# Performance work log

Measured on AMD Instinct MI355X. Metric: run time of the kernel, lower is better.

Reference implementation:

```python
import jax, jax.numpy as jnp
import numpy as np

B, S, H = 2, 2048, 2048
NH, NKV, HD = 32, 4, 128
THETA = 1e6
EPS = 1e-6


def setup_inputs() -> dict:
    key = jax.random.key(0)
    ks = jax.random.split(key, 6)
    scale = 0.02
    hidden_states = jax.random.normal(ks[0], (B, S, H), jnp.float32)
    attention_mask = jnp.broadcast_to(jnp.tril(jnp.ones((S, S), bool))[None, None], (B, 1, S, S))
    position_ids = jnp.broadcast_to(jnp.arange(S, dtype=jnp.int32), (B, S))
    Wq = jax.random.normal(ks[1], (H, NH * HD), jnp.float32) * scale
    Wk = jax.random.normal(ks[2], (H, NKV * HD), jnp.float32) * scale
    Wv = jax.random.normal(ks[3], (H, NKV * HD), jnp.float32) * scale
    Wo = jax.random.normal(ks[4], (NH * HD, H), jnp.float32) * scale
    q_norm_w = jnp.ones((HD,), jnp.float32)
    k_norm_w = jnp.ones((HD,), jnp.float32)
    return dict(hidden_states=hidden_states, attention_mask=attention_mask,
                position_ids=position_ids, Wq=Wq, Wk=Wk, Wv=Wv, Wo=Wo,
                q_norm_w=q_norm_w, k_norm_w=k_norm_w)


def _rms_norm(x, w):
    # per-head RMSNorm over last dim (head_dim)
    var = jnp.mean(x * x, axis=-1, keepdims=True)
    return x * jax.lax.rsqrt(var + EPS) * w


def _rotate_half(x):
    x1, x2 = jnp.split(x, 2, axis=-1)
    return jnp.concatenate([-x2, x1], axis=-1)


def _rope(position_ids):
    inv_freq = 1.0 / (THETA ** (jnp.arange(0, HD, 2, dtype=jnp.float32) / HD))  # [HD/2]
    freqs = position_ids.astype(jnp.float32)[..., None] * inv_freq  # [B,S,HD/2]
    emb = jnp.concatenate([freqs, freqs], axis=-1)  # [B,S,HD]
    return jnp.cos(emb), jnp.sin(emb)


def reference(hidden_states, attention_mask, position_ids, Wq, Wk, Wv, Wo, q_norm_w, k_norm_w):
    cos, sin = _rope(position_ids)               # [B,S,HD]
    cos = cos[:, :, None, :]                     # [B,S,1,HD] broadcast over heads
    sin = sin[:, :, None, :]

    q = (hidden_states @ Wq).reshape(B, S, NH, HD)
    k = (hidden_states @ Wk).reshape(B, S, NKV, HD)
    v = (hidden_states @ Wv).reshape(B, S, NKV, HD)

    q = _rms_norm(q, q_norm_w)
    k = _rms_norm(k, k_norm_w)

    q = q * cos + _rotate_half(q) * sin
    k = k * cos + _rotate_half(k) * sin

    # GQA: repeat each kv head NH//NKV times (matches HF repeat_kv ordering)
    k = jnp.repeat(k, NH // NKV, axis=2)         # [B,S,NH,HD]
    v = jnp.repeat(v, NH // NKV, axis=2)

    q = q.transpose(0, 2, 1, 3)                  # [B,NH,S,HD]
    k = k.transpose(0, 2, 1, 3)
    v = v.transpose(0, 2, 1, 3)

    scores = jnp.einsum('bhqd,bhkd->bhqk', q, k) * (HD ** -0.5)
    scores = jnp.where(attention_mask, scores, jnp.finfo(scores.dtype).min)
    attn = jax.nn.softmax(scores, axis=-1)
    ctx = jnp.einsum('bhqk,bhkd->bhqd', attn, v)  # [B,NH,S,HD]
    ctx = ctx.transpose(0, 2, 1, 3).reshape(B, S, NH * HD)
    return ctx @ Wo                               # [B,S,H]
```

## Files before the change

### kernel.cpp

```cpp
#include <hip/hip_runtime.h>
#include <stdint.h>
#include <stddef.h>

typedef unsigned short ushort_t;
typedef unsigned int uint32;

typedef _Float16 half8 __attribute__((ext_vector_type(8)));
typedef _Float16 half4 __attribute__((ext_vector_type(4)));
typedef float f32x4 __attribute__((ext_vector_type(4)));

#define NLINV (-0.2158673600755816f)
#define INV2PI 0.15915494309189535f
#define TWOPI 6.283185307179586f
#define FPITCH 40

#define GLDS(gptr, lptr)                                                                   \
  __builtin_amdgcn_global_load_lds((const __attribute__((address_space(1))) unsigned int*)(gptr), \
                                   (__attribute__((address_space(3))) unsigned int*)(lptr), \
                                   16, 0, 0)

static __device__ __forceinline__ float bf_lo(uint32 u) { union { uint32 u; float f; } v; v.u = u << 16; return v.f; }
static __device__ __forceinline__ float bf_hi(uint32 u) { union { uint32 u; float f; } v; v.u = u & 0xffff0000u; return v.f; }
static __device__ __forceinline__ ushort_t f2bf(float f) {
  union { float f; uint32 u; } v; v.f = f;
  return (ushort_t)((v.u + 0x7fffu + ((v.u >> 16) & 1u)) >> 16);
}
static __device__ __forceinline__ half8 cvt8(uint4 u) {
  half8 h;
  h[0] = (_Float16)bf_lo(u.x); h[1] = (_Float16)bf_hi(u.x);
  h[2] = (_Float16)bf_lo(u.y); h[3] = (_Float16)bf_hi(u.y);
  h[4] = (_Float16)bf_lo(u.z); h[5] = (_Float16)bf_hi(u.z);
  h[6] = (_Float16)bf_lo(u.w); h[7] = (_Float16)bf_hi(u.w);
  return h;
}
static __device__ __forceinline__ half8 load8h(const void* p, int mode, size_t eidx) {
  if (mode == 2) return ((const half8*)p)[eidx >> 3];
  if (mode == 1) {
    const float4* q = (const float4*)p + (eidx >> 2);
    const float4 a = q[0], b = q[1];
    half8 h;
    h[0] = (_Float16)a.x; h[1] = (_Float16)a.y; h[2] = (_Float16)a.z; h[3] = (_Float16)a.w;
    h[4] = (_Float16)b.x; h[5] = (_Float16)b.y; h[6] = (_Float16)b.z; h[7] = (_Float16)b.w;
    return h;
  }
  return cvt8(((const uint4*)p)[eidx >> 3]);
}
static __device__ __forceinline__ float wval(const void* w, int is_f32, int i) {
  if (is_f32) return ((const float*)w)[i];
  union { uint32 u; float f; } v; v.u = ((uint32)((const ushort_t*)w)[i]) << 16; return v.f;
}
static __device__ __forceinline__ int probe_f32(const void* p) {
  const uint32 u = ((const uint32*)p)[threadIdx.x & 63];
  const int e = (u >> 7) & 0xff;
  return __popcll(__ballot(e >= 110 && e <= 135)) < 32 ? 1 : 0;
}

__global__ __launch_bounds__(256) void probe_fill(uint32* out, uint32 pat, int nwords) {
  for (int i = blockIdx.x * 256 + threadIdx.x; i < nwords; i += gridDim.x * 256) out[i] = pat;
}

__global__ __launch_bounds__(256) void convert_hs(const void* __restrict__ hs,
                                                  _Float16* __restrict__ hsF, int n8) {
  const int f = probe_f32(hs);
  for (int i = blockIdx.x * 256 + threadIdx.x; i < n8; i += gridDim.x * 256)
    ((half8*)hsF)[i] = load8h(hs, f, (size_t)i << 3);
}

__global__ __launch_bounds__(256) void transpose_w(const void* __restrict__ W, int K, int N,
                                                   _Float16* __restrict__ Wt) {
  __shared__ __align__(16) _Float16 T[64][72];
  const int fw = probe_f32(W);
  const int n0 = blockIdx.x * 64, k0 = blockIdx.y * 64;
  const int tid = threadIdx.x;
  const int r = tid >> 2, cc = (tid & 3) * 16;
  const size_t src = (size_t)(k0 + r) * N + n0 + cc;
  const half8 v0 = load8h(W, fw, src);
  const half8 v1 = load8h(W, fw, src + 8);
  *(half8*)&T[r][cc] = v0;
  *(half8*)&T[r][cc + 8] = v1;
  __syncthreads();
  half8 o0, o1;
#pragma unroll
  for (int j = 0; j < 8; ++j) { o0[j] = T[cc + j][r]; o1[j] = T[cc + 8 + j][r]; }
  _Float16* dst = Wt + (size_t)(n0 + r) * K + k0 + cc;
  *(half8*)dst = o0;
  *(half8*)(dst + 8) = o1;
}


__global__ __launch_bounds__(256) void gemm2_rope(const _Float16* __restrict__ Af, int lda,
                                                  int arow0, const _Float16* __restrict__ Bt,
                                                  int ldb, _Float16* __restrict__ C, int ldc,
                                                  int K, const void* __restrict__ w) {
  __shared__ __align__(16) _Float16 As[128 * 32];
  __shared__ __align__(16) _Float16 Bs[128 * 32];
  __shared__ float Ct[64 * 128];
  const int fw = probe_f32(w);
  const int tid = threadIdx.x;
  const int wave = tid >> 6, lane = tid & 63;
  const int m0 = blockIdx.y * 128, n0 = blockIdx.x * 128;
  const int wm = (wave >> 1) * 64, wn = (wave & 1) * 64;
  const int fr = lane & 15, quad = lane >> 4;
  const int r0 = wave * 32 + (lane >> 2);
  const int r1 = r0 + 16;
  const int cs0 = ((lane & 3) ^ ((r0 >> 1) & 3)) << 3;
  const int cs1 = ((lane & 3) ^ ((r1 >> 1) & 3)) << 3;
  const _Float16* Ar0 = Af + (size_t)(arow0 + m0 + r0) * lda + cs0;
  const _Float16* Ar1 = Af + (size_t)(arow0 + m0 + r1) * lda + cs1;
  const _Float16* Br0 = Bt + (size_t)(n0 + r0) * ldb + cs0;
  const _Float16* Br1 = Bt + (size_t)(n0 + r1) * ldb + cs1;
  _Float16* lA0 = &As[(wave * 32) * 32];
  _Float16* lA1 = &As[(wave * 32 + 16) * 32];
  _Float16* lB0 = &Bs[(wave * 32) * 32];
  _Float16* lB1 = &Bs[(wave * 32 + 16) * 32];
  f32x4 acc[4][4] = {};
  for (int k0 = 0; k0 < K; k0 += 32) {
    __syncthreads();
    GLDS(Ar0 + k0, lA0);
    GLDS(Ar1 + k0, lA1);
    GLDS(Br0 + k0, lB0);
    GLDS(Br1 + k0, lB1);
    __syncthreads();
    half8 a[4], b[4];
#pragma unroll
    for (int t = 0; t < 4; ++t) {
      const int row = wm + t * 16 + fr;
      a[t] = *(const half8*)&As[row * 32 + ((quad ^ ((row >> 1) & 3)) << 3)];
    }
#pragma unroll
    for (int t = 0; t < 4; ++t) {
      const int row = wn + t * 16 + fr;
      b[t] = *(const half8*)&Bs[row * 32 + ((quad ^ ((row >> 1) & 3)) << 3)];
    }
#pragma unroll
    for (int mt = 0; mt < 4; ++mt)
#pragma unroll
      for (int nt = 0; nt < 4; ++nt)
        acc[mt][nt] = __builtin_amdgcn_mfma_f32_16x16x32_f16(a[mt], b[nt], acc[mt][nt], 0, 0, 0);
  }
  __syncthreads();
#pragma unroll
  for (int hf = 0; hf < 2; ++hf) {
    if ((wave >> 1) == hf) {
#pragma unroll
      for (int mt = 0; mt < 4; ++mt)
#pragma unroll
        for (int nt = 0; nt < 4; ++nt)
#pragma unroll
          for (int r = 0; r < 4; ++r)
            Ct[(mt * 16 + quad * 4 + r) * 128 + wn + nt * 16 + fr] = acc[mt][nt][r];
    }
    __syncthreads();
    const int row = tid >> 2, sub = tid & 3;
    float ss = 0.f;
#pragma unroll
    for (int j = 0; j < 32; ++j) {
      const float v = Ct[row * 128 + sub * 32 + j];
      ss += v * v;
    }
    ss += __shfl_xor(ss, 1);
    ss += __shfl_xor(ss, 2);
    const float rinv = rsqrtf(ss * (1.0f / 128.0f) + 1e-6f);
    const int grow = m0 + hf * 64 + row;
    const int s = (arow0 + grow) & 2047;
    uint32 obuf[16];
#pragma unroll
    for (int j = 0; j < 32; j += 2) {
      float o2[2];
#pragma unroll
      for (int e = 0; e < 2; ++e) {
        const int c = sub * 32 + j + e;
        const float x = Ct[row * 128 + c];
        const float p = Ct[row * 128 + (c ^ 64)];
        const float xn = x * rinv * wval(w, fw, c);
        const float pn = p * rinv * wval(w, fw, c ^ 64);
        const float rot = (c < 64) ? -pn : pn;
        const float fq = __expf((float)(c & 63) * NLINV);
        float rev = (float)s * fq * INV2PI;
        rev -= rintf(rev);
        float sn, cs;
        __sincosf(rev * TWOPI, &sn, &cs);
        o2[e] = xn * cs + rot * sn;
      }
      union { _Float16 h[2]; uint32 u; } pk;
      pk.h[0] = (_Float16)o2[0]; pk.h[1] = (_Float16)o2[1];
      obuf[j >> 1] = pk.u;
    }
    uint32* dst = (uint32*)(C + (size_t)grow * ldc + n0 + sub * 32);
#pragma unroll
    for (int j2 = 0; j2 < 16; ++j2) dst[j2] = obuf[j2];
    __syncthreads();
  }
}

__global__ __launch_bounds__(256) void gemm2_plain(const _Float16* __restrict__ Af, int lda,
                                                   int arow0, const _Float16* __restrict__ Bt,
                                                   int ldb, char* __restrict__ obase,
                                                   size_t oeoff, int ldc, int omode, int K,
                                                   const void* __restrict__ pES) {
  __shared__ __align__(16) _Float16 As[128 * 32];
  __shared__ __align__(16) _Float16 Bs[128 * 32];
  const int fes = probe_f32(pES);
  const int tid = threadIdx.x;
  const int wave = tid >> 6, lane = tid & 63;
  const int m0 = blockIdx.y * 128, n0 = blockIdx.x * 128;
  const int wm = (wave >> 1) * 64, wn = (wave & 1) * 64;
  const int fr = lane & 15, quad = lane >> 4;
  const int r0 = wave * 32 + (lane >> 2);
  const int r1 = r0 + 16;
  const int cs0 = ((lane & 3) ^ ((r0 >> 1) & 3)) << 3;
  const int cs1 = ((lane & 3) ^ ((r1 >> 1) & 3)) << 3;
  const _Float16* Ar0 = Af + (size_t)(arow0 + m0 + r0) * lda + cs0;
  const _Float16* Ar1 = Af + (size_t)(arow0 + m0 + r1) * lda + cs1;
  const _Float16* Br0 = Bt + (size_t)(n0 + r0) * ldb + cs0;
  const _Float16* Br1 = Bt + (size_t)(n0 + r1) * ldb + cs1;
  _Float16* lA0 = &As[(wave * 32) * 32];
  _Float16* lA1 = &As[(wave * 32 + 16) * 32];
  _Float16* lB0 = &Bs[(wave * 32) * 32];
  _Float16* lB1 = &Bs[(wave * 32 + 16) * 32];
  f32x4 acc[4][4] = {};
  for (int k0 = 0; k0 < K; k0 += 32) {
    __syncthreads();
    GLDS(Ar0 + k0, lA0);
    GLDS(Ar1 + k0, lA1);
    GLDS(Br0 + k0, lB0);
    GLDS(Br1 + k0, lB1);
    __syncthreads();
    half8 a[4], b[4];
#pragma unroll
    for (int t = 0; t < 4; ++t) {
      const int row = wm + t * 16 + fr;
      a[t] = *(const half8*)&As[row * 32 + ((quad ^ ((row >> 1) & 3)) << 3)];
    }
#pragma unroll
    for (int t = 0; t < 4; ++t) {
      const int row = wn + t * 16 + fr;
      b[t] = *(const half8*)&Bs[row * 32 + ((quad ^ ((row >> 1) & 3)) << 3)];
    }
#pragma unroll
    for (int mt = 0; mt < 4; ++mt)
#pragma unroll
      for (int nt = 0; nt < 4; ++nt)
        acc[mt][nt] = __builtin_amdgcn_mfma_f32_16x16x32_f16(a[mt], b[nt], acc[mt][nt], 0, 0, 0);
  }
  if (omode == 2) {
#pragma unroll
    for (int mt = 0; mt < 4; ++mt)
#pragma unroll
      for (int nt = 0; nt < 4; ++nt) {
        half4 pk;
#pragma unroll
        for (int r = 0; r < 4; ++r) pk[r] = (_Float16)acc[mt][nt][r];
        *(half4*)((_Float16*)obase + (size_t)(n0 + wn + nt * 16 + fr) * ldc +
                  m0 + wm + mt * 16 + quad * 4) = pk;
      }
    return;
  }
#pragma unroll
  for (int mt = 0; mt < 4; ++mt)
#pragma unroll
    for (int nt = 0; nt < 4; ++nt)
#pragma unroll
      for (int r = 0; r < 4; ++r) {
        const size_t idx = (size_t)(m0 + wm + mt * 16 + quad * 4 + r) * ldc + n0 + wn + nt * 16 + fr;
        const float v = acc[mt][nt][r];
        if (fes) ((float*)obase)[oeoff + idx] = v;
        else ((ushort_t*)obase)[oeoff + idx] = f2bf(v);
      }
}

__global__ __launch_bounds__(256) void gemm_rope_fast(const void* __restrict__ Araw, int lda,
                                                      int arow0, const _Float16* __restrict__ Bt,
                                                      int ldb, char* __restrict__ obase,
                                                      size_t oeoff, int ldc, int K,
                                                      const void* __restrict__ w) {
  __shared__ __align__(16) _Float16 As[128 * FPITCH];
  __shared__ __align__(16) _Float16 Bs[128 * FPITCH];
  __shared__ float Ct[64 * 128];
  const int fa = probe_f32(Araw);
  const int fw = probe_f32(w);
  _Float16* Cv = (_Float16*)(obase + oeoff * (fa ? 4u : 2u));
  const int tid = threadIdx.x;
  const int wave = tid >> 6, lane = tid & 63;
  const int m0 = blockIdx.y * 128, n0 = blockIdx.x * 128;
  const int wm = (wave >> 1) * 64, wn = (wave & 1) * 64;
  const int fr = lane & 15, quad = lane >> 4;
  const int sr = tid >> 1, sc = (tid & 1) * 16;
  f32x4 acc[4][4] = {};
  for (int k0 = 0; k0 < K; k0 += 32) {
    const size_t aidx = (size_t)(arow0 + m0 + sr) * lda + k0 + sc;
    const half8 av0 = load8h(Araw, fa, aidx);
    const half8 av1 = load8h(Araw, fa, aidx + 8);
    const _Float16* bp = Bt + (size_t)(n0 + sr) * ldb + k0 + sc;
    const half8 bv0 = *(const half8*)bp;
    const half8 bv1 = *(const half8*)(bp + 8);
    __syncthreads();
    *(half8*)&As[sr * FPITCH + sc] = av0;
    *(half8*)&As[sr * FPITCH + sc + 8] = av1;
    *(half8*)&Bs[sr * FPITCH + sc] = bv0;
    *(half8*)&Bs[sr * FPITCH + sc + 8] = bv1;
    __syncthreads();
    half8 a[4], b[4];
#pragma unroll
    for (int t = 0; t < 4; ++t)
      a[t] = *(const half8*)&As[(wm + t * 16 + fr) * FPITCH + quad * 8];
#pragma unroll
    for (int t = 0; t < 4; ++t)
      b[t] = *(const half8*)&Bs[(wn + t * 16 + fr) * FPITCH + quad * 8];
#pragma unroll
    for (int mt = 0; mt < 4; ++mt)
#pragma unroll
      for (int nt = 0; nt < 4; ++nt)
        acc[mt][nt] = __builtin_amdgcn_mfma_f32_16x16x32_f16(a[mt], b[nt], acc[mt][nt], 0, 0, 0);
  }
  __syncthreads();
#pragma unroll
  for (int hf = 0; hf < 2; ++hf) {
    if ((wave >> 1) == hf) {
#pragma unroll
      for (int mt = 0; mt < 4; ++mt)
#pragma unroll
        for (int nt = 0; nt < 4; ++nt)
#pragma unroll
          for (int r = 0; r < 4; ++r)
            Ct[(mt * 16 + quad * 4 + r) * 128 + wn + nt * 16 + fr] = acc[mt][nt][r];
    }
    __syncthreads();
    const int row = tid >> 2, sub = tid & 3;
    float ss = 0.f;
#pragma unroll
    for (int j = 0; j < 32; ++j) {
      const float v = Ct[row * 128 + sub * 32 + j];
      ss += v * v;
    }
    ss += __shfl_xor(ss, 1);
    ss += __shfl_xor(ss, 2);
    const float rinv = rsqrtf(ss * (1.0f / 128.0f) + 1e-6f);
    const int grow = m0 + hf * 64 + row;
    const int s = (arow0 + grow) & 2047;
    uint32 obuf[16];
#pragma unroll
    for (int j = 0; j < 32; j += 2) {
      float o2[2];
#pragma unroll
      for (int e = 0; e < 2; ++e) {
        const int c = sub * 32 + j + e;
        const float x = Ct[row * 128 + c];
        const float p = Ct[row * 128 + (c ^ 64)];
        const float xn = x * rinv * wval(w, fw, c);
        const float pn = p * rinv * wval(w, fw, c ^ 64);
        const float rot = (c < 64) ? -pn : pn;
        const float fq = __expf((float)(c & 63) * NLINV);
        float rev = (float)s * fq * INV2PI;
        rev -= rintf(rev);
        float sn, cs;
        __sincosf(rev * TWOPI, &sn, &cs);
        o2[e] = xn * cs + rot * sn;
      }
      union { _Float16 h[2]; uint32 u; } pk;
      pk.h[0] = (_Float16)o2[0]; pk.h[1] = (_Float16)o2[1];
      obuf[j >> 1] = pk.u;
    }
    uint32* dst = (uint32*)(Cv + (size_t)grow * ldc + n0 + sub * 32);
#pragma unroll
    for (int j2 = 0; j2 < 16; ++j2) dst[j2] = obuf[j2];
    __syncthreads();
  }
}

__global__ __launch_bounds__(256) void gemm_plain_fast(const char* __restrict__ abase, size_t aeoff,
                                                       int lda, int amode, int arow0,
                                                       const _Float16* __restrict__ Bt, int ldb,
                                                       char* __restrict__ obase, size_t oeoff,
                                                       int ldc, int omode, int K,
                                                       const void* __restrict__ pES) {
  __shared__ __align__(16) _Float16 As[128 * FPITCH];
  __shared__ __align__(16) _Float16 Bs[128 * FPITCH];
  const int fes = probe_f32(pES);
  const uint32 es = fes ? 4u : 2u;
  const void* A = abase + aeoff * es;
  const int fa = (amode == 2) ? 2 : probe_f32(abase);
  const int tid = threadIdx.x;
  const int wave = tid >> 6, lane = tid & 63;
  const int m0 = blockIdx.y * 128, n0 = blockIdx.x * 128;
  const int wm = (wave >> 1) * 64, wn = (wave & 1) * 64;
  const int fr = lane & 15, quad = lane >> 4;
  const int sr = tid >> 1, sc = (tid & 1) * 16;
  f32x4 acc[4][4] = {};
  for (int k0 = 0; k0 < K; k0 += 32) {
    const size_t aidx = (size_t)(arow0 + m0 + sr) * lda + k0 + sc;
    const half8 av0 = load8h(A, fa, aidx);
    const half8 av1 = load8h(A, fa, aidx + 8);
    const _Float16* bp = Bt + (size_t)(n0 + sr) * ldb + k0 + sc;
    const half8 bv0 = *(const half8*)bp;
    const half8 bv1 = *(const half8*)(bp + 8);
    __syncthreads();
    *(half8*)&As[sr * FPITCH + sc] = av0;
    *(half8*)&As[sr * FPITCH + sc + 8] = av1;
    *(half8*)&Bs[sr * FPITCH + sc] = bv0;
    *(half8*)&Bs[sr * FPITCH + sc + 8] = bv1;
    __syncthreads();
    half8 a[4], b[4];
#pragma unroll
    for (int t = 0; t < 4; ++t)
      a[t] = *(const half8*)&As[(wm + t * 16 + fr) * FPITCH + quad * 8];
#pragma unroll
    for (int t = 0; t < 4; ++t)
      b[t] = *(const half8*)&Bs[(wn + t * 16 + fr) * FPITCH + quad * 8];
#pragma unroll
    for (int mt = 0; mt < 4; ++mt)
#pragma unroll
      for (int nt = 0; nt < 4; ++nt)
        acc[mt][nt] = __builtin_amdgcn_mfma_f32_16x16x32_f16(a[mt], b[nt], acc[mt][nt], 0, 0, 0);
  }
  if (omode == 2) {
#pragma unroll
    for (int mt = 0; mt < 4; ++mt)
#pragma unroll
      for (int nt = 0; nt < 4; ++nt) {
        half4 pk;
#pragma unroll
        for (int r = 0; r < 4; ++r) pk[r] = (_Float16)acc[mt][nt][r];
        *(half4*)((_Float16*)obase + (size_t)(n0 + wn + nt * 16 + fr) * ldc +
                  m0 + wm + mt * 16 + quad * 4) = pk;
      }
    return;
  }
#pragma unroll
  for (int mt = 0; mt < 4; ++mt)
#pragma unroll
    for (int nt = 0; nt < 4; ++nt)
#pragma unroll
      for (int r = 0; r < 4; ++r) {
        const size_t idx = (size_t)(m0 + wm + mt * 16 + quad * 4 + r) * ldc + n0 + wn + nt * 16 + fr;
        const float v = acc[mt][nt][r];
        if (omode == 1) ((_Float16*)obase)[idx] = (_Float16)v;
        else if (fes) ((float*)obase)[oeoff + idx] = v;
        else ((ushort_t*)obase)[oeoff + idx] = f2bf(v);
      }
}

#define LOADKV(J0)                                                                             \
  {                                                                                            \
    _Pragma("unroll") for (int ii = 0; ii < 4; ++ii) {                                         \
      const int i = tid + ii * 256;                                                            \
      const int r = i >> 4, c = i & 15;                                                        \
      kreg[ii] = *(const half8*)(Kb + (size_t)((J0) + r) * 512 + kv * 128 + ((c ^ (r & 7)) << 3)); \
      const int d = i >> 3, c2 = i & 7;                                                        \
      vreg[ii] = *(const half8*)(Vb + (size_t)(kv * 128 + d) * 2048 + (J0) + ((c2 ^ (d & 7)) << 3)); \
    }                                                                                          \
  }

__global__ __launch_bounds__(256, 2) void attn_fwd(char* __restrict__ qbase, size_t qeoff,
                                                   const _Float16* __restrict__ Kb,
                                                   const _Float16* __restrict__ Vb, int c0,
                                                   const void* __restrict__ pES) {
  __shared__ __align__(16) _Float16 Ks[64 * 128];
  __shared__ __align__(16) _Float16 Vt[128 * 64];
  __shared__ __align__(16) _Float16 Ps[4 * 16 * 64];
  const uint32 es = probe_f32(pES) ? 4u : 2u;
  _Float16* Qbuf = (_Float16*)(qbase + qeoff * es);
  const int tid = threadIdx.x;
  const int wave = tid >> 6, lane = tid & 63;
  const int fr = lane & 15, quad = lane >> 4;
  const int h = blockIdx.y, kv = h >> 3;
  const int qb0 = blockIdx.x * 64;
  const int qg = c0 + qb0;
  const int qrow0 = qb0 + wave * 16;
  _Float16* Pw = &Ps[wave * 1024];
  half8 qa[4];
#pragma unroll
  for (int kt = 0; kt < 4; ++kt)
    qa[kt] = *(const half8*)(Qbuf + (size_t)(qrow0 + fr) * 4096 + h * 128 + kt * 32 + quad * 8);
  f32x4 Oa[8];
#pragma unroll
  for (int dt = 0; dt < 8; ++dt) Oa[dt] = (f32x4)0.f;
  float mr[4], lr[4];
#pragma unroll
  for (int r = 0; r < 4; ++r) { mr[r] = -1e30f; lr[r] = 0.f; }
  const int ntiles = qg / 64 + 1;
  half8 kreg[4], vreg[4];
  LOADKV(0);
  for (int t = 0; t < ntiles; ++t) {
    __syncthreads();
#pragma unroll
    for (int ii = 0; ii < 4; ++ii) {
      *(half8*)&Ks[(tid + ii * 256) * 8] = kreg[ii];
      *(half8*)&Vt[(tid + ii * 256) * 8] = vreg[ii];
    }
    __syncthreads();
    if (t + 1 < ntiles) LOADKV((t + 1) * 64);
    f32x4 s[4];
#pragma unroll
    for (int nt = 0; nt < 4; ++nt) s[nt] = (f32x4)0.f;
#pragma unroll
    for (int kt = 0; kt < 4; ++kt)
#pragma unroll
      for (int nt = 0; nt < 4; ++nt) {
        const int row = nt * 16 + fr;
        const int boff = ((row << 8) + ((kt * 32 + quad * 8) << 1)) ^ ((row & 7) << 4);
        const half8 kb = *(const half8*)((const char*)Ks + boff);
        s[nt] = __builtin_amdgcn_mfma_f32_16x16x32_f16(qa[kt], kb, s[nt], 0, 0, 0);
      }
    const float SC = 0.08838834764831845f;
    const int j0 = t * 64;
    if (t == ntiles - 1) {
#pragma unroll
      for (int nt = 0; nt < 4; ++nt)
#pragma unroll
        for (int r = 0; r < 4; ++r) {
          const int kpos = j0 + nt * 16 + fr;
          const int qpos = qg + wave * 16 + quad * 4 + r;
          s[nt][r] = (kpos > qpos) ? -1e30f : s[nt][r] * SC;
        }
    } else {
#pragma unroll
      for (int nt = 0; nt < 4; ++nt)
#pragma unroll
        for (int r = 0; r < 4; ++r) s[nt][r] *= SC;
    }
    float al[4];
#pragma unroll
    for (int r = 0; r < 4; ++r) {
      float mx = fmaxf(fmaxf(s[0][r], s[1][r]), fmaxf(s[2][r], s[3][r]));
      mx = fmaxf(mx, __shfl_xor(mx, 1));
      mx = fmaxf(mx, __shfl_xor(mx, 2));
      mx = fmaxf(mx, __shfl_xor(mx, 4));
      mx = fmaxf(mx, __shfl_xor(mx, 8));
      const float mn = fmaxf(mr[r], mx);
      al[r] = __expf(mr[r] - mn);
      mr[r] = mn;
    }
    float rs[4] = {0.f, 0.f, 0.f, 0.f};
#pragma unroll
    for (int nt = 0; nt < 4; ++nt)
#pragma unroll
      for (int r = 0; r < 4; ++r) {
        const float p = __expf(s[nt][r] - mr[r]);
        rs[r] += p;
        const int q = quad * 4 + r;
        const int boff = (((q << 7) + ((nt * 16 + fr) << 1)) ^ ((q & 7) << 4));
        *(_Float16*)((char*)Pw + boff) = (_Float16)p;
      }
#pragma unroll
    for (int r = 0; r < 4; ++r) {
      rs[r] += __shfl_xor(rs[r], 1);
      rs[r] += __shfl_xor(rs[r], 2);
      rs[r] += __shfl_xor(rs[r], 4);
      rs[r] += __shfl_xor(rs[r], 8);
      lr[r] = lr[r] * al[r] + rs[r];
    }
#pragma unroll
    for (int dt = 0; dt < 8; ++dt)
#pragma unroll
      for (int r = 0; r < 4; ++r) Oa[dt][r] *= al[r];
    half8 pa[2];
#pragma unroll
    for (int kt = 0; kt < 2; ++kt) {
      const int boff = (((fr << 7) + ((kt * 32 + quad * 8) << 1)) ^ ((fr & 7) << 4));
      pa[kt] = *(const half8*)((const char*)Pw + boff);
    }
#pragma unroll
    for (int dt = 0; dt < 8; ++dt)
#pragma unroll
      for (int kt = 0; kt < 2; ++kt) {
        const int d = dt * 16 + fr;
        const int boff = (((d << 7) + ((kt * 32 + quad * 8) << 1)) ^ ((d & 7) << 4));
        const half8 vb = *(const half8*)((const char*)Vt + boff);
        Oa[dt] = __builtin_amdgcn_mfma_f32_16x16x32_f16(pa[kt], vb, Oa[dt], 0, 0, 0);
      }
  }
#pragma unroll
  for (int r = 0; r < 4; ++r) {
    const float linv = 1.0f / lr[r];
    _Float16* orow = Qbuf + (size_t)(qrow0 + quad * 4 + r) * 4096 + h * 128;
#pragma unroll
    for (int dt = 0; dt < 8; ++dt) orow[dt * 16 + fr] = (_Float16)(Oa[dt][r] * linv);
  }
}

extern "C" void kernel_launch(void* const* d_in, const int* in_sizes, int n_in,
                              void* d_out, int out_size, void* d_ws, size_t ws_size,
                              hipStream_t stream) {
  (void)in_sizes; (void)n_in; (void)out_size;
  const void* hs = d_in[0];
  const void* Wq = d_in[3];
  const void* Wk = d_in[4];
  const void* Wv = d_in[5];
  const void* Wo = d_in[6];
  const void* qw = d_in[7];
  const void* kw = d_in[8];
  char* dout = (char*)d_out;
  const size_t MB = 1048576;

  probe_fill<<<2048, 256, 0, stream>>>((uint32*)d_out, 0x42C842C8u, 4194304);
  if (ws_size < 40 * MB) {
    probe_fill<<<2048, 256, 0, stream>>>((uint32*)d_out, 0x43484348u, 4194304);
    return;
  }
  _Float16* Kbuf = (_Float16*)d_ws;
  _Float16* Vbuf = (_Float16*)((char*)d_ws + 2 * MB);
  _Float16* WqT = (_Float16*)((char*)d_ws + 4 * MB);
  _Float16* WoT = (_Float16*)((char*)d_ws + 20 * MB);
  _Float16* WkT = (_Float16*)((char*)d_ws + 36 * MB);
  _Float16* WvT = (_Float16*)((char*)d_ws + 38 * MB);
  const size_t QOFF = 4194304;

  transpose_w<<<dim3(64, 32), 256, 0, stream>>>(Wq, 2048, 4096, WqT);
  transpose_w<<<dim3(8, 32), 256, 0, stream>>>(Wk, 2048, 512, WkT);
  transpose_w<<<dim3(8, 32), 256, 0, stream>>>(Wv, 2048, 512, WvT);
  transpose_w<<<dim3(32, 64), 256, 0, stream>>>(Wo, 4096, 2048, WoT);

  if (ws_size >= 72 * MB) {
    char* Qw = (char*)d_ws + 40 * MB;
    _Float16* hsF = (_Float16*)((char*)d_ws + 56 * MB);
    convert_hs<<<2048, 256, 0, stream>>>(hs, hsF, 1048576);
    for (int b = 0; b < 2; ++b) {
      gemm2_rope<<<dim3(4, 16), 256, 0, stream>>>(hsF, 2048, b * 2048, WkT, 2048,
                                                  Kbuf, 512, 2048, kw);
      gemm2_plain<<<dim3(4, 16), 256, 0, stream>>>(hsF, 2048, b * 2048, WvT, 2048,
                                                   (char*)Vbuf, 0, 2048, 2, 2048, hs);
      gemm2_rope<<<dim3(32, 16), 256, 0, stream>>>(hsF, 2048, b * 2048, WqT, 2048,
                                                   (_Float16*)Qw, 4096, 2048, qw);
      attn_fwd<<<dim3(32, 32), 256, 0, stream>>>(Qw, 0, Kbuf, Vbuf, 0, hs);
      gemm2_plain<<<dim3(16, 16), 256, 0, stream>>>((const _Float16*)Qw, 4096, 0, WoT, 4096,
                                                    dout, (size_t)b * 4194304, 2048, 0, 4096, hs);
    }
    return;
  }

  if (ws_size >= 56 * MB) {
    char* Qw = (char*)d_ws + 40 * MB;
    for (int b = 0; b < 2; ++b) {
      gemm_rope_fast<<<dim3(4, 16), 256, 0, stream>>>(hs, 2048, b * 2048, WkT, 2048,
                                                      (char*)Kbuf, 0, 512, 2048, kw);
      gemm_plain_fast<<<dim3(4, 16), 256, 0, stream>>>((const char*)hs, 0, 2048, 0, b * 2048,
                                                       WvT, 2048, (char*)Vbuf, 0, 2048, 2,
                                                       2048, hs);
      gemm_rope_fast<<<dim3(32, 16), 256, 0, stream>>>(hs, 2048, b * 2048, WqT, 2048,
                                                       Qw, 0, 4096, 2048, qw);
      attn_fwd<<<dim3(32, 32), 256, 0, stream>>>(Qw, 0, Kbuf, Vbuf, 0, hs);
      gemm_plain_fast<<<dim3(16, 16), 256, 0, stream>>>((const char*)Qw, 0, 4096, 2, 0,
                                                        WoT, 4096, dout,
                                                        (size_t)b * 4194304, 2048, 0, 4096, hs);
    }
    return;
  }

  for (int b = 0; b < 2; ++b) {
    gemm_rope_fast<<<dim3(4, 16), 256, 0, stream>>>(hs, 2048, b * 2048, WkT, 2048,
                                                    (char*)Kbuf, 0, 512, 2048, kw);
    gemm_plain_fast<<<dim3(4, 16), 256, 0, stream>>>((const char*)hs, 0, 2048, 0, b * 2048,
                                                     WvT, 2048, (char*)Vbuf, 0, 2048, 2,
                                                     2048, hs);
    if (b == 0) {
      for (int c0 = 0; c0 < 2048; c0 += 1024) {
        gemm_rope_fast<<<dim3(32, 8), 256, 0, stream>>>(hs, 2048, c0, WqT, 2048,
                                                        dout, QOFF, 4096, 2048, qw);
        attn_fwd<<<dim3(16, 32), 256, 0, stream>>>(dout, QOFF, Kbuf, Vbuf, c0, hs);
        gemm_plain_fast<<<dim3(16, 8), 256, 0, stream>>>((const char*)dout, QOFF, 4096, 2, 0,
                                                         WoT, 4096, dout, (size_t)c0 * 2048,
                                                         2048, 0, 4096, hs);
      }
    } else {
      const int cs[8][2] = {{1536, 512}, {1024, 512}, {768, 256}, {512, 256},
                            {384, 128}, {256, 128}, {128, 128}, {0, 128}};
      for (int i = 0; i < 8; ++i) {
        const int c0 = cs[i][0], CH = cs[i][1];
        char* qb = (c0 >= 256) ? dout : ((char*)d_ws + 262144);
        const size_t qoff = (c0 >= 256) ? QOFF : 0;
        gemm_rope_fast<<<dim3(32, CH / 128), 256, 0, stream>>>(hs, 2048, 2048 + c0, WqT, 2048,
                                                               qb, qoff, 4096, 2048, qw);
        attn_fwd<<<dim3(CH / 64, 32), 256, 0, stream>>>(qb, qoff, Kbuf, Vbuf, c0, hs);
        gemm_plain_fast<<<dim3(16, CH / 128), 256, 0, stream>>>((const char*)qb, qoff, 4096, 2,
                                                                0, WoT, 4096, dout,
                                                                (size_t)(2048 + c0) * 2048,
                                                                2048, 0, 4096, hs);
      }
    }
  }
}
```

Measured before the change: 1.129 ms.

## Restructure attention into single-wave blocks reading K/V directly from global

```diff
diff --git a/kernel.cpp b/kernel.cpp
--- a/kernel.cpp
+++ b/kernel.cpp
@@ -440,34 +440,24 @@
       }
 }
 
-#define LOADKV(J0)                                                                             \
-  {                                                                                            \
-    _Pragma("unroll") for (int ii = 0; ii < 4; ++ii) {                                         \
-      const int i = tid + ii * 256;                                                            \
-      const int r = i >> 4, c = i & 15;                                                        \
-      kreg[ii] = *(const half8*)(Kb + (size_t)((J0) + r) * 512 + kv * 128 + ((c ^ (r & 7)) << 3)); \
-      const int d = i >> 3, c2 = i & 7;                                                        \
-      vreg[ii] = *(const half8*)(Vb + (size_t)(kv * 128 + d) * 2048 + (J0) + ((c2 ^ (d & 7)) << 3)); \
-    }                                                                                          \
-  }
-
-__global__ __launch_bounds__(256, 2) void attn_fwd(char* __restrict__ qbase, size_t qeoff,
-                                                   const _Float16* __restrict__ Kb,
-                                                   const _Float16* __restrict__ Vb, int c0,
-                                                   const void* __restrict__ pES) {
-  __shared__ __align__(16) _Float16 Ks[64 * 128];
-  __shared__ __align__(16) _Float16 Vt[128 * 64];
-  __shared__ __align__(16) _Float16 Ps[4 * 16 * 64];
+__global__ __launch_bounds__(64, 3) void attn_fwd(char* __restrict__ qbase, size_t qeoff,
+                                                  const _Float16* __restrict__ Kb,
+                                                  const _Float16* __restrict__ Vb, int c0,
+                                                  const void* __restrict__ pES) {
+  __shared__ __align__(16) _Float16 Pw[16 * 64];
   const uint32 es = probe_f32(pES) ? 4u : 2u;
-  _Float16* Qbuf = (_Float16*)(qbase + qeoff * es);
-  const int tid = threadIdx.x;
-  const int wave = tid >> 6, lane = tid & 63;
+  const int z = blockIdx.z;
+  _Float16* Qbuf = (_Float16*)(qbase + qeoff * es) + (size_t)z * (2048u * 4096u);
+  const _Float16* K = Kb + (size_t)z * (2048u * 512u);
+  const _Float16* V = Vb + (size_t)z * (512u * 2048u);
+  const int lane = threadIdx.x;
   const int fr = lane & 15, quad = lane >> 4;
   const int h = blockIdx.y, kv = h >> 3;
-  const int qb0 = blockIdx.x * 64;
-  const int qg = c0 + qb0;
-  const int qrow0 = qb0 + wave * 16;
-  _Float16* Pw = &Ps[wave * 1024];
+  const int nbx = gridDim.x;
+  const int bx = blockIdx.x;
+  const int pbx = (bx & 1) ? (nbx - 1 - (bx >> 1)) : (bx >> 1);
+  const int qrow0 = pbx * 16;
+  const int qg = c0 + qrow0;
   half8 qa[4];
 #pragma unroll
   for (int kt = 0; kt < 4; ++kt)
@@ -479,38 +469,30 @@
 #pragma unroll
   for (int r = 0; r < 4; ++r) { mr[r] = -1e30f; lr[r] = 0.f; }
   const int ntiles = qg / 64 + 1;
-  half8 kreg[4], vreg[4];
-  LOADKV(0);
   for (int t = 0; t < ntiles; ++t) {
-    __syncthreads();
-#pragma unroll
-    for (int ii = 0; ii < 4; ++ii) {
-      *(half8*)&Ks[(tid + ii * 256) * 8] = kreg[ii];
-      *(half8*)&Vt[(tid + ii * 256) * 8] = vreg[ii];
-    }
-    __syncthreads();
-    if (t + 1 < ntiles) LOADKV((t + 1) * 64);
+    const int j0 = t * 64;
     f32x4 s[4];
 #pragma unroll
     for (int nt = 0; nt < 4; ++nt) s[nt] = (f32x4)0.f;
 #pragma unroll
-    for (int kt = 0; kt < 4; ++kt)
-#pragma unroll
-      for (int nt = 0; nt < 4; ++nt) {
-        const int row = nt * 16 + fr;
-        const int boff = ((row << 8) + ((kt * 32 + quad * 8) << 1)) ^ ((row & 7) << 4);
-        const half8 kb = *(const half8*)((const char*)Ks + boff);
-        s[nt] = __builtin_amdgcn_mfma_f32_16x16x32_f16(qa[kt], kb, s[nt], 0, 0, 0);
-      }
+    for (int kt = 0; kt < 4; ++kt) {
+      half8 kb[4];
+#pragma unroll
+      for (int nt = 0; nt < 4; ++nt)
+        kb[nt] = *(const half8*)(K + (size_t)(j0 + nt * 16 + fr) * 512 + kv * 128 +
+                                 kt * 32 + quad * 8);
+#pragma unroll
+      for (int nt = 0; nt < 4; ++nt)
+        s[nt] = __builtin_amdgcn_mfma_f32_16x16x32_f16(qa[kt], kb[nt], s[nt], 0, 0, 0);
+    }
     const float SC = 0.08838834764831845f;
-    const int j0 = t * 64;
     if (t == ntiles - 1) {
 #pragma unroll
       for (int nt = 0; nt < 4; ++nt)
 #pragma unroll
         for (int r = 0; r < 4; ++r) {
           const int kpos = j0 + nt * 16 + fr;
-          const int qpos = qg + wave * 16 + quad * 4 + r;
+          const int qpos = qg + quad * 4 + r;
           s[nt][r] = (kpos > qpos) ? -1e30f : s[nt][r] * SC;
         }
     } else {
@@ -561,14 +543,16 @@
       pa[kt] = *(const half8*)((const char*)Pw + boff);
     }
 #pragma unroll
-    for (int dt = 0; dt < 8; ++dt)
-#pragma unroll
-      for (int kt = 0; kt < 2; ++kt) {
-        const int d = dt * 16 + fr;
-        const int boff = (((d << 7) + ((kt * 32 + quad * 8) << 1)) ^ ((d & 7) << 4));
-        const half8 vb = *(const half8*)((const char*)Vt + boff);
-        Oa[dt] = __builtin_amdgcn_mfma_f32_16x16x32_f16(pa[kt], vb, Oa[dt], 0, 0, 0);
-      }
+    for (int kt = 0; kt < 2; ++kt) {
+      half8 vb[8];
+#pragma unroll
+      for (int dt = 0; dt < 8; ++dt)
+        vb[dt] = *(const half8*)(V + (size_t)(kv * 128 + dt * 16 + fr) * 2048 + j0 +
+                                 kt * 32 + quad * 8);
+#pragma unroll
+      for (int dt = 0; dt < 8; ++dt)
+        Oa[dt] = __builtin_amdgcn_mfma_f32_16x16x32_f16(pa[kt], vb[dt], Oa[dt], 0, 0, 0);
+    }
   }
 #pragma unroll
   for (int r = 0; r < 4; ++r) {
@@ -598,6 +582,38 @@
     probe_fill<<<2048, 256, 0, stream>>>((uint32*)d_out, 0x43484348u, 4194304);
     return;
   }
+
+  if (ws_size >= 92 * MB) {
+    _Float16* Kb2 = (_Float16*)d_ws;
+    _Float16* Vb2 = (_Float16*)((char*)d_ws + 4 * MB);
+    _Float16* WqT = (_Float16*)((char*)d_ws + 8 * MB);
+    _Float16* WoT = (_Float16*)((char*)d_ws + 24 * MB);
+    _Float16* WkT = (_Float16*)((char*)d_ws + 40 * MB);
+    _Float16* WvT = (_Float16*)((char*)d_ws + 42 * MB);
+    _Float16* Qw2 = (_Float16*)((char*)d_ws + 44 * MB);
+    _Float16* hsF = (_Float16*)((char*)d_ws + 76 * MB);
+    transpose_w<<<dim3(64, 32), 256, 0, stream>>>(Wq, 2048, 4096, WqT);
+    transpose_w<<<dim3(8, 32), 256, 0, stream>>>(Wk, 2048, 512, WkT);
+    transpose_w<<<dim3(8, 32), 256, 0, stream>>>(Wv, 2048, 512, WvT);
+    transpose_w<<<dim3(32, 64), 256, 0, stream>>>(Wo, 4096, 2048, WoT);
+    convert_hs<<<2048, 256, 0, stream>>>(hs, hsF, 1048576);
+    for (int b = 0; b < 2; ++b) {
+      gemm2_rope<<<dim3(4, 16), 256, 0, stream>>>(hsF, 2048, b * 2048, WkT, 2048,
+                                                  Kb2 + (size_t)b * 1048576, 512, 2048, kw);
+      gemm2_plain<<<dim3(4, 16), 256, 0, stream>>>(hsF, 2048, b * 2048, WvT, 2048,
+                                                   (char*)(Vb2 + (size_t)b * 1048576), 0, 2048,
+                                                   2, 2048, hs);
+      gemm2_rope<<<dim3(32, 16), 256, 0, stream>>>(hsF, 2048, b * 2048, WqT, 2048,
+                                                   Qw2 + (size_t)b * 8388608, 4096, 2048, qw);
+    }
+    attn_fwd<<<dim3(128, 32, 2), 64, 0, stream>>>((char*)Qw2, 0, Kb2, Vb2, 0, hs);
+    for (int b = 0; b < 2; ++b)
+      gemm2_plain<<<dim3(16, 16), 256, 0, stream>>>(Qw2 + (size_t)b * 8388608, 4096, 0,
+                                                    WoT, 4096, dout, (size_t)b * 4194304, 2048,
+                                                    0, 4096, hs);
+    return;
+  }
+
   _Float16* Kbuf = (_Float16*)d_ws;
   _Float16* Vbuf = (_Float16*)((char*)d_ws + 2 * MB);
   _Float16* WqT = (_Float16*)((char*)d_ws + 4 * MB);
@@ -622,7 +638,7 @@
                                                    (char*)Vbuf, 0, 2048, 2, 2048, hs);
       gemm2_rope<<<dim3(32, 16), 256, 0, stream>>>(hsF, 2048, b * 2048, WqT, 2048,
                                                    (_Float16*)Qw, 4096, 2048, qw);
-      attn_fwd<<<dim3(32, 32), 256, 0, stream>>>(Qw, 0, Kbuf, Vbuf, 0, hs);
+      attn_fwd<<<dim3(128, 32), 64, 0, stream>>>(Qw, 0, Kbuf, Vbuf, 0, hs);
       gemm2_plain<<<dim3(16, 16), 256, 0, stream>>>((const _Float16*)Qw, 4096, 0, WoT, 4096,
                                                     dout, (size_t)b * 4194304, 2048, 0, 4096, hs);
     }
@@ -639,7 +655,7 @@
                                                        2048, hs);
       gemm_rope_fast<<<dim3(32, 16), 256, 0, stream>>>(hs, 2048, b * 2048, WqT, 2048,
                                                        Qw, 0, 4096, 2048, qw);
-      attn_fwd<<<dim3(32, 32), 256, 0, stream>>>(Qw, 0, Kbuf, Vbuf, 0, hs);
+      attn_fwd<<<dim3(128, 32), 64, 0, stream>>>(Qw, 0, Kbuf, Vbuf, 0, hs);
       gemm_plain_fast<<<dim3(16, 16), 256, 0, stream>>>((const char*)Qw, 0, 4096, 2, 0,
                                                         WoT, 4096, dout,
                                                         (size_t)b * 4194304, 2048, 0, 4096, hs);
@@ -657,7 +673,7 @@
       for (int c0 = 0; c0 < 2048; c0 += 1024) {
         gemm_rope_fast<<<dim3(32, 8), 256, 0, stream>>>(hs, 2048, c0, WqT, 2048,
                                                         dout, QOFF, 4096, 2048, qw);
-        attn_fwd<<<dim3(16, 32), 256, 0, stream>>>(dout, QOFF, Kbuf, Vbuf, c0, hs);
+        attn_fwd<<<dim3(64, 32), 64, 0, stream>>>(dout, QOFF, Kbuf, Vbuf, c0, hs);
         gemm_plain_fast<<<dim3(16, 8), 256, 0, stream>>>((const char*)dout, QOFF, 4096, 2, 0,
                                                          WoT, 4096, dout, (size_t)c0 * 2048,
                                                          2048, 0, 4096, hs);
@@ -671,7 +687,7 @@
         const size_t qoff = (c0 >= 256) ? QOFF : 0;
         gemm_rope_fast<<<dim3(32, CH / 128), 256, 0, stream>>>(hs, 2048, 2048 + c0, WqT, 2048,
                                                                qb, qoff, 4096, 2048, qw);
-        attn_fwd<<<dim3(CH / 64, 32), 256, 0, stream>>>(qb, qoff, Kbuf, Vbuf, c0, hs);
+        attn_fwd<<<dim3(CH / 16, 32), 64, 0, stream>>>(qb, qoff, Kbuf, Vbuf, c0, hs);
         gemm_plain_fast<<<dim3(16, CH / 128), 256, 0, stream>>>((const char*)qb, qoff, 4096, 2,
                                                                 0, WoT, 4096, dout,
                                                                 (size_t)(2048 + c0) * 2048,
```

After: 1.600 ms. 41.7% more time.

## Batch attention across both batches in one launch with causal load-balanced block order

Applied to the files above, without the earlier changes.

```diff
diff --git a/kernel.cpp b/kernel.cpp
--- a/kernel.cpp
+++ b/kernel.cpp
@@ -445,9 +445,9 @@
     _Pragma("unroll") for (int ii = 0; ii < 4; ++ii) {                                         \
       const int i = tid + ii * 256;                                                            \
       const int r = i >> 4, c = i & 15;                                                        \
-      kreg[ii] = *(const half8*)(Kb + (size_t)((J0) + r) * 512 + kv * 128 + ((c ^ (r & 7)) << 3)); \
+      kreg[ii] = *(const half8*)(K + (size_t)((J0) + r) * 512 + kv * 128 + ((c ^ (r & 7)) << 3)); \
       const int d = i >> 3, c2 = i & 7;                                                        \
-      vreg[ii] = *(const half8*)(Vb + (size_t)(kv * 128 + d) * 2048 + (J0) + ((c2 ^ (d & 7)) << 3)); \
+      vreg[ii] = *(const half8*)(V + (size_t)(kv * 128 + d) * 2048 + (J0) + ((c2 ^ (d & 7)) << 3)); \
     }                                                                                          \
   }
 
@@ -459,12 +459,18 @@
   __shared__ __align__(16) _Float16 Vt[128 * 64];
   __shared__ __align__(16) _Float16 Ps[4 * 16 * 64];
   const uint32 es = probe_f32(pES) ? 4u : 2u;
-  _Float16* Qbuf = (_Float16*)(qbase + qeoff * es);
+  const int z = blockIdx.z;
+  _Float16* Qbuf = (_Float16*)(qbase + qeoff * es) + (size_t)z * (2048u * 4096u);
+  const _Float16* K = Kb + (size_t)z * (2048u * 512u);
+  const _Float16* V = Vb + (size_t)z * (512u * 2048u);
   const int tid = threadIdx.x;
   const int wave = tid >> 6, lane = tid & 63;
   const int fr = lane & 15, quad = lane >> 4;
   const int h = blockIdx.y, kv = h >> 3;
-  const int qb0 = blockIdx.x * 64;
+  const int nbx = gridDim.x;
+  const int bx = blockIdx.x;
+  const int pbx = (bx & 1) ? (nbx - 1 - (bx >> 1)) : (bx >> 1);
+  const int qb0 = pbx * 64;
   const int qg = c0 + qb0;
   const int qrow0 = qb0 + wave * 16;
   _Float16* Pw = &Ps[wave * 1024];
@@ -598,6 +604,38 @@
     probe_fill<<<2048, 256, 0, stream>>>((uint32*)d_out, 0x43484348u, 4194304);
     return;
   }
+
+  if (ws_size >= 92 * MB) {
+    _Float16* Kb2 = (_Float16*)d_ws;
+    _Float16* Vb2 = (_Float16*)((char*)d_ws + 4 * MB);
+    _Float16* WqT = (_Float16*)((char*)d_ws + 8 * MB);
+    _Float16* WoT = (_Float16*)((char*)d_ws + 24 * MB);
+    _Float16* WkT = (_Float16*)((char*)d_ws + 40 * MB);
+    _Float16* WvT = (_Float16*)((char*)d_ws + 42 * MB);
+    _Float16* Qw2 = (_Float16*)((char*)d_ws + 44 * MB);
+    _Float16* hsF = (_Float16*)((char*)d_ws + 76 * MB);
+    transpose_w<<<dim3(64, 32), 256, 0, stream>>>(Wq, 2048, 4096, WqT);
+    transpose_w<<<dim3(8, 32), 256, 0, stream>>>(Wk, 2048, 512, WkT);
+    transpose_w<<<dim3(8, 32), 256, 0, stream>>>(Wv, 2048, 512, WvT);
+    transpose_w<<<dim3(32, 64), 256, 0, stream>>>(Wo, 4096, 2048, WoT);
+    convert_hs<<<2048, 256, 0, stream>>>(hs, hsF, 1048576);
+    for (int b = 0; b < 2; ++b) {
+      gemm2_rope<<<dim3(4, 16), 256, 0, stream>>>(hsF, 2048, b * 2048, WkT, 2048,
+                                                  Kb2 + (size_t)b * 1048576, 512, 2048, kw);
+      gemm2_plain<<<dim3(4, 16), 256, 0, stream>>>(hsF, 2048, b * 2048, WvT, 2048,
+                                                   (char*)(Vb2 + (size_t)b * 1048576), 0, 2048,
+                                                   2, 2048, hs);
+      gemm2_rope<<<dim3(32, 16), 256, 0, stream>>>(hsF, 2048, b * 2048, WqT, 2048,
+                                                   Qw2 + (size_t)b * 8388608, 4096, 2048, qw);
+    }
+    attn_fwd<<<dim3(32, 32, 2), 256, 0, stream>>>((char*)Qw2, 0, Kb2, Vb2, 0, hs);
+    for (int b = 0; b < 2; ++b)
+      gemm2_plain<<<dim3(16, 16), 256, 0, stream>>>(Qw2 + (size_t)b * 8388608, 4096, 0,
+                                                    WoT, 4096, dout, (size_t)b * 4194304, 2048,
+                                                    0, 4096, hs);
+    return;
+  }
+
   _Float16* Kbuf = (_Float16*)d_ws;
   _Float16* Vbuf = (_Float16*)((char*)d_ws + 2 * MB);
   _Float16* WqT = (_Float16*)((char*)d_ws + 4 * MB);
```

After: 1.128 ms. No clear change (-0.1%).
